# Kernel tuning notes

Measured on AMD Instinct MI355X. Metric: run time of the kernel, lower is better.

Reference implementation:

```python
import jax, jax.numpy as jnp
import numpy as np

K = 7  # kernel_size
D = 2  # dilation


def window_start(idx, L, K, D):
    """NATTEN neighborhood window start (clamped at borders, dilation-group aware)."""
    nh = K // 2
    if D <= 1:
        return jnp.maximum(idx - nh, 0) + jnp.where(idx + nh >= L, L - idx - nh - 1, 0)
    ni = idx - nh * D
    imodd = idx % D
    a = (L // D) * D
    b = L - a
    right = jnp.where(imodd < b, L - b + imodd - 2 * nh * D, a + imodd - K * D)
    return jnp.where(ni < 0, imodd, jnp.where(idx + nh * D >= L, right, ni))


def setup_inputs() -> dict:
    key = jax.random.key(0)
    ks = jax.random.split(key, 7)
    B, Cin, H, W, Cout = 2, 128, 112, 112, 64
    x = jax.random.normal(ks[0], (B, Cin, H, W), dtype=jnp.float32)
    Wq = jax.random.normal(ks[1], (Cout, Cin), dtype=jnp.float32) * 0.02
    Wk = jax.random.normal(ks[2], (Cout, Cin), dtype=jnp.float32) * 0.02
    Wv = jax.random.normal(ks[3], (Cout, Cin), dtype=jnp.float32) * 0.02
    bq = jax.random.normal(ks[4], (Cout,), dtype=jnp.float32) * 0.02
    bk = jax.random.normal(ks[5], (Cout,), dtype=jnp.float32) * 0.02
    bv = jax.random.normal(ks[6], (Cout,), dtype=jnp.float32) * 0.02
    return {"x": x, "Wq": Wq, "bq": bq, "Wk": Wk, "bk": bk, "Wv": Wv, "bv": bv}


def reference(x, Wq, bq, Wk, bk, Wv, bv):
    B, Cin, H, W = x.shape
    # 1x1 conv projections -> channels-last [B, H, W, C]
    q = jnp.einsum('bchw,oc->bhwo', x, Wq) + bq
    k = jnp.einsum('bchw,oc->bhwo', x, Wk) + bk
    v = jnp.einsum('bchw,oc->bhwo', x, Wv) + bv
    C = q.shape[-1]
    scale = jnp.asarray(C, q.dtype) ** -0.5  # NATTEN default scale (heads=1, head_dim=C)

    offs = jnp.arange(K) * D
    ih = window_start(jnp.arange(H), H, K, D)[:, None] + offs  # [H, K]
    iw = window_start(jnp.arange(W), W, K, D)[:, None] + offs  # [W, K]
    # gather neighborhoods -> [B, H, W, K, K, C]
    idx_h = ih[:, None, :, None]  # [H,1,K,1]
    idx_w = iw[None, :, None, :]  # [1,W,1,K]
    kw = k[:, idx_h, idx_w, :]
    vw = v[:, idx_h, idx_w, :]

    scores = jnp.einsum('bhwc,bhwijc->bhwij', q * scale, kw)  # [B,H,W,K,K]
    attn = jax.nn.softmax(scores.reshape(B, H, W, K * K), axis=-1)
    out = jnp.einsum('bhwn,bhwnc->bhwc', attn, vw.reshape(B, H, W, K * K, C))
    return out.transpose(0, 3, 1, 2)  # [B, C, H, W]
```

## Files before the change

kernel.cpp:

```cpp
#include <hip/hip_runtime.h>
#include <hip/hip_bf16.h>

#define HWSZ 12544
#define WDIM 112
#define CIN  128
#define NPIX 25088
#define VTROW 6272
#define VTOFF (2 * (size_t)NPIX * 64)

typedef __attribute__((ext_vector_type(8))) short          short8;
typedef __attribute__((ext_vector_type(4))) float          float4v;
typedef __attribute__((ext_vector_type(4))) unsigned short ushort4v;

__device__ __forceinline__ int window_start7x2(int idx, int L) {
    int ni = idx - 6;
    int imodd = idx & 1;
    int a = (L >> 1) << 1;
    int bb = L - a;
    int right = (imodd < bb) ? (L - bb + imodd - 12) : (a + imodd - 14);
    if (ni < 0) return imodd;
    if (idx + 6 >= L) return right;
    return ni;
}

__device__ __forceinline__ unsigned short f2bf(float f) {
    __hip_bfloat16 h = __float2bfloat16(f);
    return *(unsigned short*)&h;
}

__global__ __launch_bounds__(256) void proj_mfma(
    const float* __restrict__ x,
    const float* __restrict__ Wq, const float* __restrict__ bq,
    const float* __restrict__ Wk, const float* __restrict__ bk,
    const float* __restrict__ Wv, const float* __restrict__ bv,
    unsigned short* __restrict__ qbuf)
{
    __shared__ __align__(16) unsigned short wsb[64][136];
    __shared__ __align__(16) unsigned short trans[64 * 80];

    const int t = threadIdx.x, lane = t & 63, wv = t >> 6, quad = lane >> 4;
    const int col = lane & 15;

    const int bx   = blockIdx.x;
    const int tile = (bx / 24) * 8 + (bx & 7);
    const int m    = (bx >> 3) % 3;

    const float* Wm = (m == 0) ? Wq : (m == 1) ? Wk : Wv;
    const float* bm = (m == 0) ? bq : (m == 1) ? bk : bv;

    const int pix0 = tile * 64;
    const int b    = tile / 196;
    const int hw0  = pix0 - b * HWSZ;
    const float* xb = x + (size_t)b * CIN * HWSZ;

    #pragma unroll
    for (int i = 0; i < 8; ++i) {
        int u = t + 256 * i;
        int o = u >> 5, cq = (u & 31) * 4;
        float4 w4 = *(const float4*)&Wm[o * 128 + cq];
        ushort4v s4 = { f2bf(w4.x), f2bf(w4.y), f2bf(w4.z), f2bf(w4.w) };
        *(ushort4v*)&wsb[o][cq] = s4;
    }

    const int hwpx = hw0 + wv * 16 + col;
    short8 af[4];
    #pragma unroll
    for (int kc = 0; kc < 4; ++kc) {
        #pragma unroll
        for (int j = 0; j < 8; ++j) {
            int c = kc * 32 + quad * 8 + j;
            af[kc][j] = (short)f2bf(xb[(size_t)c * HWSZ + hwpx]);
        }
    }
    __syncthreads();

    float4v acc[4] = {{0,0,0,0},{0,0,0,0},{0,0,0,0},{0,0,0,0}};
    #pragma unroll
    for (int kc = 0; kc < 4; ++kc) {
        #pragma unroll
        for (int nt = 0; nt < 4; ++nt) {
            short8 bf = *(const short8*)&wsb[nt * 16 + col][kc * 32 + quad * 8];
            acc[nt] = __builtin_amdgcn_mfma_f32_16x16x32_bf16(af[kc], bf, acc[nt], 0, 0, 0);
        }
    }
    __syncthreads();

    if (m < 2) {
        const float scale = (m == 0) ? 0.125f : 1.0f;
        #pragma unroll
        for (int nt = 0; nt < 4; ++nt) {
            float bias = bm[nt * 16 + col];
            #pragma unroll
            for (int r = 0; r < 4; ++r) {
                int px = wv * 16 + quad * 4 + r;
                trans[px * 80 + nt * 16 + col] = f2bf((acc[nt][r] + bias) * scale);
            }
        }
        __syncthreads();
        unsigned short* outm = qbuf + (size_t)m * NPIX * 64;
        const int tpx = t >> 2, chunk = t & 3;
        const unsigned short* src = &trans[tpx * 80 + chunk * 16];
        unsigned short* dst = outm + (size_t)(pix0 + tpx) * 64 + chunk * 16;
        *(short8*)(dst)     = *(const short8*)(src);
        *(short8*)(dst + 8) = *(const short8*)(src + 8);
    } else {
        #pragma unroll
        for (int nt = 0; nt < 4; ++nt) {
            int ch = nt * 16 + col;
            float bias = bm[ch];
            #pragma unroll
            for (int r = 0; r < 4; ++r) {
                int px = wv * 16 + quad * 4 + r;
                trans[ch * 80 + (px & 1) * 40 + (px >> 1)] = f2bf(acc[nt][r] + bias);
            }
        }
        __syncthreads();
        unsigned short* vt = qbuf + VTOFF;
        const int ch = t >> 2, parity = (t >> 1) & 1, half = t & 1;
        const unsigned short* src = &trans[ch * 80 + parity * 40 + half * 16];
        unsigned short* dst = vt + (size_t)((b * 2 + parity) * 64 + ch) * VTROW
                            + (hw0 >> 1) + half * 16;
        *(short8*)(dst)     = *(const short8*)(src);
        *(short8*)(dst + 8) = *(const short8*)(src + 8);
    }
}

__global__ __launch_bounds__(128) void attn_mfma(
    const unsigned short* __restrict__ qkv, float* __restrict__ out)
{
    __shared__ __align__(16) unsigned short ps[2][16 * 232];
    __shared__ __align__(16) float lds_out[64 * 36];

    const int lane = threadIdx.x & 63, g = threadIdx.x >> 6;
    const int quad = lane >> 4, col = lane & 15;

    const int bx   = blockIdx.x;
    const int xcd  = bx & 7;
    const int idx  = bx >> 3;
    const int h    = xcd * 14 + (idx >> 3);
    const int b    = (idx >> 2) & 1;
    const int sub  = idx & 3;
    const int pb   = (sub < 3) ? sub * 16 : 40;

    const int hs  = window_start7x2(h, WDIM);
    const int ws0 = window_start7x2(2 * pb + g, WDIM);
    const int cb0 = (ws0 >> 1) & ~7;
    const int pixbase = b * HWSZ;

    const unsigned short* qg = qkv;
    const unsigned short* kg = qkv + (size_t)NPIX * 64;
    const unsigned short* vt = qkv + VTOFF + (size_t)(b * 2 + g) * 64 * VTROW;

    const int qpix = pixbase + h * WDIM + 2 * (pb + col) + g;
    short8 af0 = *(const short8*)(qg + (size_t)qpix * 64 + quad * 8);
    short8 af1 = *(const short8*)(qg + (size_t)qpix * 64 + 32 + quad * 8);

    int cbr[4];
    #pragma unroll
    for (int r = 0; r < 4; ++r)
        cbr[r] = (window_start7x2(2 * (pb + quad * 4 + r) + g, WDIM) >> 1) - cb0;

    int rowoff[7];
    #pragma unroll
    for (int kc = 0; kc < 7; ++kc) {
        int u8 = kc * 32 + quad * 8;
        rowoff[kc] = (hs + 2 * (u8 >> 5)) * 56 + cb0 + (u8 & 31);
    }
    short8 vpre[4][4];
    #pragma unroll
    for (int kc = 0; kc < 4; ++kc)
        #pragma unroll
        for (int nt = 0; nt < 4; ++nt)
            vpre[kc][nt] = *(const short8*)
                (vt + (size_t)(nt * 16 + col) * VTROW + rowoff[kc]);

    float4v S[14];
    #pragma unroll
    for (int nt = 0; nt < 14; ++nt) {
        int u = nt * 16 + col;
        int i = u >> 5, c = u & 31;
        int wcol = cb0 + c;
        int kw = 2 * wcol + g; kw = (kw > 111) ? 111 : kw;
        int kp = pixbase + (hs + 2 * i) * WDIM + kw;
        float4v a = {0, 0, 0, 0};
        a = __builtin_amdgcn_mfma_f32_16x16x32_bf16(
                af0, *(const short8*)(kg + (size_t)kp * 64 + quad * 8), a, 0, 0, 0);
        a = __builtin_amdgcn_mfma_f32_16x16x32_bf16(
                af1, *(const short8*)(kg + (size_t)kp * 64 + 32 + quad * 8), a, 0, 0, 0);
        bool colok = (wcol <= 55);
        #pragma unroll
        for (int r = 0; r < 4; ++r) {
            bool valid = colok && ((unsigned)(c - cbr[r]) < 7u);
            S[nt][r] = valid ? a[r] : -1e30f;
        }
    }

    #pragma unroll
    for (int r = 0; r < 4; ++r) {
        float sum = 0.0f;
        #pragma unroll
        for (int nt = 0; nt < 14; ++nt) {
            float e = __expf(S[nt][r]);
            S[nt][r] = e;
            sum += e;
        }
        #pragma unroll
        for (int msk = 1; msk < 16; msk <<= 1)
            sum += __shfl_xor(sum, msk, 64);
        float rinv = 1.0f / sum;
        int row = quad * 4 + r;
        #pragma unroll
        for (int nt = 0; nt < 14; ++nt)
            ps[g][row * 232 + nt * 16 + col] = f2bf(S[nt][r] * rinv);
    }

    float4v O[4] = {{0,0,0,0},{0,0,0,0},{0,0,0,0},{0,0,0,0}};
    #pragma unroll
    for (int kc = 0; kc < 4; ++kc) {
        short8 pa = *(const short8*)&ps[g][col * 232 + kc * 32 + quad * 8];
        #pragma unroll
        for (int nt = 0; nt < 4; ++nt)
            O[nt] = __builtin_amdgcn_mfma_f32_16x16x32_bf16(pa, vpre[kc][nt], O[nt], 0, 0, 0);
    }
    #pragma unroll
    for (int kc = 4; kc < 7; ++kc) {
        short8 pa = *(const short8*)&ps[g][col * 232 + kc * 32 + quad * 8];
        #pragma unroll
        for (int nt = 0; nt < 4; ++nt) {
            short8 vb = *(const short8*)(vt + (size_t)(nt * 16 + col) * VTROW + rowoff[kc]);
            O[nt] = __builtin_amdgcn_mfma_f32_16x16x32_bf16(pa, vb, O[nt], 0, 0, 0);
        }
    }

    #pragma unroll
    for (int nt = 0; nt < 4; ++nt) {
        int ch = nt * 16 + col;
        #pragma unroll
        for (int r = 0; r < 4; ++r)
            lds_out[ch * 36 + 2 * (quad * 4 + r) + g] = O[nt][r];
    }
    __syncthreads();

    {
        const int ch = threadIdx.x >> 1, half = threadIdx.x & 1;
        float* ob = out + (size_t)(b * 64 + ch) * HWSZ + h * WDIM + 2 * pb + half * 16;
        const float* src = &lds_out[ch * 36 + half * 16];
        #pragma unroll
        for (int j = 0; j < 4; ++j)
            *(float4*)(ob + j * 4) = *(const float4*)(src + j * 4);
    }
}

extern "C" void kernel_launch(void* const* d_in, const int* in_sizes, int n_in,
                              void* d_out, int out_size, void* d_ws, size_t ws_size,
                              hipStream_t stream) {
    const float* x  = (const float*)d_in[0];
    const float* Wq = (const float*)d_in[1];
    const float* bq = (const float*)d_in[2];
    const float* Wk = (const float*)d_in[3];
    const float* bk = (const float*)d_in[4];
    const float* Wv = (const float*)d_in[5];
    const float* bv = (const float*)d_in[6];
    float* out = (float*)d_out;

    unsigned short* qkv = (unsigned short*)d_ws;

    proj_mfma<<<dim3(1176), dim3(256), 0, stream>>>(x, Wq, bq, Wk, bk, Wv, bv, qkv);
    attn_mfma<<<dim3(896), dim3(128), 0, stream>>>(qkv, out);
}
```

Measured before the change: 94.82 us.

## Compute Q, K, V projections in one block per tile; add MFMA priority hints

```diff
diff --git a/kernel.cpp b/kernel.cpp
--- a/kernel.cpp
+++ b/kernel.cpp
@@ -35,31 +35,29 @@
     const float* __restrict__ Wv, const float* __restrict__ bv,
     unsigned short* __restrict__ qbuf)
 {
-    __shared__ __align__(16) unsigned short wsb[64][136];
+    __shared__ __align__(16) unsigned short wsb[3][64][136];
     __shared__ __align__(16) unsigned short trans[64 * 80];
 
     const int t = threadIdx.x, lane = t & 63, wv = t >> 6, quad = lane >> 4;
     const int col = lane & 15;
 
-    const int bx   = blockIdx.x;
-    const int tile = (bx / 24) * 8 + (bx & 7);
-    const int m    = (bx >> 3) % 3;
-
-    const float* Wm = (m == 0) ? Wq : (m == 1) ? Wk : Wv;
-    const float* bm = (m == 0) ? bq : (m == 1) ? bk : bv;
-
+    const int tile = blockIdx.x;
     const int pix0 = tile * 64;
     const int b    = tile / 196;
     const int hw0  = pix0 - b * HWSZ;
     const float* xb = x + (size_t)b * CIN * HWSZ;
 
     #pragma unroll
-    for (int i = 0; i < 8; ++i) {
-        int u = t + 256 * i;
-        int o = u >> 5, cq = (u & 31) * 4;
-        float4 w4 = *(const float4*)&Wm[o * 128 + cq];
-        ushort4v s4 = { f2bf(w4.x), f2bf(w4.y), f2bf(w4.z), f2bf(w4.w) };
-        *(ushort4v*)&wsb[o][cq] = s4;
+    for (int m = 0; m < 3; ++m) {
+        const float* Wm = (m == 0) ? Wq : (m == 1) ? Wk : Wv;
+        #pragma unroll
+        for (int i = 0; i < 8; ++i) {
+            int u = t + 256 * i;
+            int o = u >> 5, cq = (u & 31) * 4;
+            float4 w4 = *(const float4*)&Wm[o * 128 + cq];
+            ushort4v s4 = { f2bf(w4.x), f2bf(w4.y), f2bf(w4.z), f2bf(w4.w) };
+            *(ushort4v*)&wsb[m][o][cq] = s4;
+        }
     }
 
     const int hwpx = hw0 + wv * 16 + col;
@@ -74,26 +72,37 @@
     }
     __syncthreads();
 
-    float4v acc[4] = {{0,0,0,0},{0,0,0,0},{0,0,0,0},{0,0,0,0}};
+    float4v acc[3][4];
+    #pragma unroll
+    for (int m = 0; m < 3; ++m)
+        #pragma unroll
+        for (int nt = 0; nt < 4; ++nt)
+            acc[m][nt] = (float4v){0, 0, 0, 0};
+
     #pragma unroll
     for (int kc = 0; kc < 4; ++kc) {
         #pragma unroll
-        for (int nt = 0; nt < 4; ++nt) {
-            short8 bf = *(const short8*)&wsb[nt * 16 + col][kc * 32 + quad * 8];
-            acc[nt] = __builtin_amdgcn_mfma_f32_16x16x32_bf16(af[kc], bf, acc[nt], 0, 0, 0);
+        for (int m = 0; m < 3; ++m) {
+            #pragma unroll
+            for (int nt = 0; nt < 4; ++nt) {
+                short8 bfv = *(const short8*)&wsb[m][nt * 16 + col][kc * 32 + quad * 8];
+                acc[m][nt] = __builtin_amdgcn_mfma_f32_16x16x32_bf16(af[kc], bfv, acc[m][nt], 0, 0, 0);
+            }
         }
     }
     __syncthreads();
 
-    if (m < 2) {
+    #pragma unroll
+    for (int m = 0; m < 2; ++m) {
         const float scale = (m == 0) ? 0.125f : 1.0f;
+        const float* bm = (m == 0) ? bq : bk;
         #pragma unroll
         for (int nt = 0; nt < 4; ++nt) {
             float bias = bm[nt * 16 + col];
             #pragma unroll
             for (int r = 0; r < 4; ++r) {
                 int px = wv * 16 + quad * 4 + r;
-                trans[px * 80 + nt * 16 + col] = f2bf((acc[nt][r] + bias) * scale);
+                trans[px * 80 + nt * 16 + col] = f2bf((acc[m][nt][r] + bias) * scale);
             }
         }
         __syncthreads();
@@ -103,15 +112,18 @@
         unsigned short* dst = outm + (size_t)(pix0 + tpx) * 64 + chunk * 16;
         *(short8*)(dst)     = *(const short8*)(src);
         *(short8*)(dst + 8) = *(const short8*)(src + 8);
-    } else {
+        __syncthreads();
+    }
+
+    {
         #pragma unroll
         for (int nt = 0; nt < 4; ++nt) {
             int ch = nt * 16 + col;
-            float bias = bm[ch];
+            float bias = bv[ch];
             #pragma unroll
             for (int r = 0; r < 4; ++r) {
                 int px = wv * 16 + quad * 4 + r;
-                trans[ch * 80 + (px & 1) * 40 + (px >> 1)] = f2bf(acc[nt][r] + bias);
+                trans[ch * 80 + (px & 1) * 40 + (px >> 1)] = f2bf(acc[2][nt][r] + bias);
             }
         }
         __syncthreads();
@@ -183,10 +195,12 @@
         int kw = 2 * wcol + g; kw = (kw > 111) ? 111 : kw;
         int kp = pixbase + (hs + 2 * i) * WDIM + kw;
         float4v a = {0, 0, 0, 0};
+        __builtin_amdgcn_s_setprio(1);
         a = __builtin_amdgcn_mfma_f32_16x16x32_bf16(
                 af0, *(const short8*)(kg + (size_t)kp * 64 + quad * 8), a, 0, 0, 0);
         a = __builtin_amdgcn_mfma_f32_16x16x32_bf16(
                 af1, *(const short8*)(kg + (size_t)kp * 64 + 32 + quad * 8), a, 0, 0, 0);
+        __builtin_amdgcn_s_setprio(0);
         bool colok = (wcol <= 55);
         #pragma unroll
         for (int r = 0; r < 4; ++r) {
@@ -218,9 +232,11 @@
     #pragma unroll
     for (int kc = 0; kc < 4; ++kc) {
         short8 pa = *(const short8*)&ps[g][col * 232 + kc * 32 + quad * 8];
+        __builtin_amdgcn_s_setprio(1);
         #pragma unroll
         for (int nt = 0; nt < 4; ++nt)
             O[nt] = __builtin_amdgcn_mfma_f32_16x16x32_bf16(pa, vpre[kc][nt], O[nt], 0, 0, 0);
+        __builtin_amdgcn_s_setprio(0);
     }
     #pragma unroll
     for (int kc = 4; kc < 7; ++kc) {
@@ -228,7 +244,9 @@
         #pragma unroll
         for (int nt = 0; nt < 4; ++nt) {
             short8 vb = *(const short8*)(vt + (size_t)(nt * 16 + col) * VTROW + rowoff[kc]);
+            __builtin_amdgcn_s_setprio(1);
             O[nt] = __builtin_amdgcn_mfma_f32_16x16x32_bf16(pa, vb, O[nt], 0, 0, 0);
+            __builtin_amdgcn_s_setprio(0);
         }
     }
 
@@ -265,6 +283,6 @@
 
     unsigned short* qkv = (unsigned short*)d_ws;
 
-    proj_mfma<<<dim3(1176), dim3(256), 0, stream>>>(x, Wq, bq, Wk, bk, Wv, bv, qkv);
+    proj_mfma<<<dim3(392), dim3(256), 0, stream>>>(x, Wq, bq, Wk, bk, Wv, bv, qkv);
     attn_mfma<<<dim3(896), dim3(128), 0, stream>>>(qkv, out);
 }
```

Measured after the change: 95.56 us. About the same (+0.8%).
